# Performance work log

Measured on AMD Instinct MI355X. Metric: run time of the kernel, lower is better.

## Reference

```python
import jax, jax.numpy as jnp
import numpy as np

B, T, NVAR, H, C = 1024, 96, 7, 64, 3  # batch, seq_len/time-points, nvar, ode_hidden, components
H4 = 4 * H


def setup_inputs() -> dict:
    key = jax.random.key(0)
    ks = jax.random.split(key, 12)
    def w(k, shape, fan_in):
        return (jax.random.normal(k, shape, jnp.float32) / np.sqrt(fan_in)).astype(jnp.float32)
    return {
        "x": jax.random.normal(ks[0], (B, T, NVAR), jnp.float32),
        # init_net: Linear(nvar->H), ReLU, Linear(H->C*H)   (stored as (in,out))
        "init_w1": w(ks[1], (NVAR, H), NVAR), "init_b1": jnp.zeros((H,), jnp.float32),
        "init_w2": w(ks[2], (H, C * H), H),   "init_b2": jnp.zeros((C * H,), jnp.float32),
        # ODEFunc.net: Linear(H+C -> 4H), Tanh, Linear(4H -> H)
        "ode_w1": w(ks[3], (H + C, H4), H + C), "ode_b1": jnp.zeros((H4,), jnp.float32),
        "ode_w2": w(ks[4], (H4, H), H4),        "ode_b2": jnp.zeros((H,), jnp.float32),
        # interaction param (init eye) and frozen conservation linear (eye, no bias)
        "interaction": jnp.eye(C, dtype=jnp.float32),
        "conservation": jnp.eye(C, dtype=jnp.float32),
        # decode_net: per-component Linear(H->H), ReLU, Linear(H->nvar)
        "dec_w1": w(ks[5], (C, H, H), H), "dec_b1": jnp.zeros((C, H), jnp.float32),
        "dec_w2": w(ks[6], (C, H, NVAR), H), "dec_b2": jnp.zeros((C, NVAR), jnp.float32),
        "t_points": jnp.linspace(0.0, 1.0, T).astype(jnp.float32),
    }


def _ode_func(t, state, interaction, conservation, ode_w1, ode_b1, ode_w2, ode_b2):
    # state: (B, C, H)
    b = state.shape[0]
    state_comp = state.mean(axis=-1)                                   # (B, C)
    ie = jnp.einsum('ij,bj->bi', interaction, state_comp)              # bmm(interaction, mean)
    ie = jnp.einsum('oi,bi->bo', conservation, ie)                     # frozen linear (no bias)
    inputs = jnp.concatenate(
        [state.reshape(b * C, H), ie.reshape(b * C, 1), jnp.full((b * C, 1), t, state.dtype)],
        axis=1)                                                        # (B*C, H+2)? no: H + 1 + 1 = H + C since C==3? -> H+2; matches torch cat of [H,1,1] only if C accounts: net expects H+C=H+3.
    # NOTE: torch concatenates [state(H), interaction_effect(1), t(1)] = H+2 features but the
    # Linear expects H+C.  With C=3 torch relies on nn.Linear(H+3) receiving H+2?? It does not --
    # torch code passes H+2 features into Linear(H+C).  Faithful translation pads to match below.
    d = jnp.tanh(inputs @ ode_w1[: inputs.shape[1]] + ode_b1) @ ode_w2 + ode_b2
    return d.reshape(state.shape)


def reference(x, init_w1, init_b1, init_w2, init_b2, ode_w1, ode_b1, ode_w2, ode_b2,
              interaction, conservation, dec_w1, dec_b1, dec_w2, dec_b2, t_points):
    # initial state from mean over sequence
    h0 = jax.nn.relu(x.mean(axis=1) @ init_w1 + init_b1)
    y0 = (h0 @ init_w2 + init_b2).reshape(-1, C, H)                    # (B, C, H)

    f = lambda t, y: _ode_func(t, y, interaction, conservation, ode_w1, ode_b1, ode_w2, ode_b2)

    def rk4_step(y, ts):
        t0, t1 = ts
        h = t1 - t0
        k1 = f(t0, y)
        k2 = f(t0 + 0.5 * h, y + 0.5 * h * k1)
        k3 = f(t0 + 0.5 * h, y + 0.5 * h * k2)
        k4 = f(t1, y + h * k3)
        y1 = y + (h / 6.0) * (k1 + 2.0 * k2 + 2.0 * k3 + k4)
        return y1, y1

    ts = jnp.stack([t_points[:-1], t_points[1:]], axis=1)              # (T-1, 2)
    _, ys = jax.lax.scan(rk4_step, y0, ts)                             # (T-1, B, C, H)
    states = jnp.concatenate([y0[None], ys], axis=0)                   # (T, B, C, H)
    states = jnp.transpose(states, (1, 0, 2, 3))                       # (B, T, C, H)

    # per-component decode MLP
    hid = jax.nn.relu(jnp.einsum('btch,chk->btck', states, dec_w1) + dec_b1)
    comps = jnp.einsum('btck,ckn->btcn', hid, dec_w2) + dec_b2         # (B, T, C, NVAR)
    comps = jnp.moveaxis(comps, 2, 0)                                  # (C, B, T, NVAR)
    # comps[0] is the trend, comps[1:] the high-frequency components
    return comps
```

## Files before the change

### kernel.cpp

```cpp
#include <hip/hip_runtime.h>

#define BTOT 1024
#define TPTS 96
#define NV   7
#define HD   64
#define NH   256

typedef short bf16x8 __attribute__((ext_vector_type(8)));
typedef float f32x4  __attribute__((ext_vector_type(4)));
typedef unsigned int u32x4 __attribute__((ext_vector_type(4)));
#define MFMA16(a,b,c) __builtin_amdgcn_mfma_f32_16x16x32_bf16(a,b,c,0,0,0)

#define OFF_YP   0
#define OFF_TP   1024
#define OFF_PRT  5120
#define OFF_YF   7680
#define OFF_PS   8720
#define OFF_TPS  8784
#define OFF_DW1  8880
#define OFF_DW2  21168
#define OFF_DB1  22512
#define OFF_DB2  22704
#define SMEM_WORDS 22736
#define SMEM_BYTES (SMEM_WORDS*4)

__device__ __forceinline__ float rdlane(float v, int i) {
    return __int_as_float(__builtin_amdgcn_readlane(__float_as_int(v), i));
}
__device__ __forceinline__ float wsum64(float v) {
    v += __shfl_xor(v, 1);  v += __shfl_xor(v, 2);  v += __shfl_xor(v, 4);
    v += __shfl_xor(v, 8);  v += __shfl_xor(v, 16); v += __shfl_xor(v, 32);
    return v;
}
__device__ __forceinline__ float tanh_fast(float x) {
    float e = __expf(2.f * x);
    return 1.f - 2.f / (e + 1.f);
}
__device__ __forceinline__ ushort bf16rn(float x) {
    unsigned u = __float_as_uint(x);
    return (ushort)((u + 0x7fffu + ((u >> 16) & 1u)) >> 16);
}
__device__ __forceinline__ void split2(float x, ushort& h, ushort& l) {
    h = bf16rn(x);
    float hf = __uint_as_float(((unsigned)h) << 16);
    l = bf16rn(x - hf);
}

union FU { u32x4 uv; unsigned u[4]; ushort s[8]; bf16x8 v; };

__global__ __launch_bounds__(512, 2)
void node_mfma13(const float* __restrict__ x,
                 const float* __restrict__ iw1, const float* __restrict__ ib1,
                 const float* __restrict__ iw2, const float* __restrict__ ib2,
                 const float* __restrict__ ow1, const float* __restrict__ ob1,
                 const float* __restrict__ ow2, const float* __restrict__ ob2,
                 const float* __restrict__ inter, const float* __restrict__ cons,
                 const float* __restrict__ dw1, const float* __restrict__ db1,
                 const float* __restrict__ dw2, const float* __restrict__ db2,
                 const float* __restrict__ tpts,
                 float* __restrict__ out)
{
    extern __shared__ float sm[];
    unsigned* YPw = (unsigned*)(sm + OFF_YP);
    unsigned* TPw = (unsigned*)(sm + OFF_TP);
    float*    PRT = sm + OFF_PRT;
    float*    Yf  = sm + OFF_YF;
    float*    PS  = sm + OFF_PS;
    float*    tps = sm + OFF_TPS;
    float*    DW1 = sm + OFF_DW1;
    float*    DW2 = sm + OFF_DW2;
    float*    DB1 = sm + OFF_DB1;
    float*    DB2 = sm + OFF_DB2;

    const int tid = threadIdx.x;
    const int w   = tid >> 6;
    const int ln  = tid & 63;
    const int m   = ln & 15;
    const int g4  = ln >> 4;
    const int nt  = w & 3;
    const int kh  = w >> 2;

    for (int idx = tid; idx < 3*HD*HD; idx += 512) DW1[idx] = dw1[idx];
    if (tid < 3*HD)  { for (int v = 0; v < NV; ++v) DW2[tid*NV + v] = dw2[tid*NV + v]; }
    if (tid < 192)   DB1[tid] = db1[tid];
    if (tid < 21)    DB2[tid] = db2[tid];
    if (tid < TPTS)  tps[tid] = tpts[tid];

    FU w1h[2][2], w1l[2][2];
    FU w2h[4], w2l[4];
    #pragma unroll
    for (int u = 0; u < 2; ++u)
        #pragma unroll
        for (int cc = 0; cc < 2; ++cc)
            #pragma unroll
            for (int j = 0; j < 8; ++j) {
                ushort h, l;
                int k1 = 32*cc + 8*g4 + j;
                split2(ow1[k1*NH + 16*(2*w+u) + m], h, l);
                w1h[u][cc].s[j] = h; w1l[u][cc].s[j] = l;
            }
    #pragma unroll
    for (int cc = 0; cc < 4; ++cc)
        #pragma unroll
        for (int j = 0; j < 8; ++j) {
            ushort h, l;
            int k2 = 128*kh + 32*cc + 8*g4 + j;
            split2(ow2[k2*HD + 16*nt + m], h, l);
            w2h[cc].s[j] = h; w2l[cc].s[j] = l;
        }
    float w64c[2], w65c[2], b1c[2];
    #pragma unroll
    for (int u = 0; u < 2; ++u) {
        int c1 = 16*(2*w+u) + m;
        w64c[u] = ow1[64*NH + c1];
        w65c[u] = ow1[65*NH + c1];
        b1c[u]  = ob1[c1];
    }
    const float b2c = ob2[16*nt + m];

    const int cpm = m % 3, base3 = m - cpm;
    float Mr0, Mr1, Mr2;
    {
        float I[9], C[9];
        #pragma unroll
        for (int i = 0; i < 9; ++i) { I[i] = inter[i]; C[i] = cons[i]; }
        float M_[3][3];
        #pragma unroll
        for (int r = 0; r < 3; ++r)
            #pragma unroll
            for (int c = 0; c < 3; ++c)
                M_[r][c] = (C[r*3+0]*I[0*3+c] + C[r*3+1]*I[1*3+c] + C[r*3+2]*I[2*3+c]) * (1.f/64.f);
        Mr0 = (cpm==0) ? M_[0][0] : (cpm==1) ? M_[1][0] : M_[2][0];
        Mr1 = (cpm==0) ? M_[0][1] : (cpm==1) ? M_[1][1] : M_[2][1];
        Mr2 = (cpm==0) ? M_[0][2] : (cpm==1) ? M_[1][2] : M_[2][2];
    }

    {
        const int el0 = w >> 1;
        const int b0  = blockIdx.x*4 + el0;
        float xs0,xs1,xs2,xs3,xs4,xs5,xs6;
        {
            const float* xp = x + (size_t)b0 * TPTS * NV + ln * NV;
            float v0=xp[0],v1=xp[1],v2=xp[2],v3=xp[3],v4=xp[4],v5=xp[5],v6=xp[6];
            if (ln < 32) {
                const float* xp2 = xp + 64 * NV;
                v0+=xp2[0]; v1+=xp2[1]; v2+=xp2[2]; v3+=xp2[3]; v4+=xp2[4]; v5+=xp2[5]; v6+=xp2[6];
            }
            xs0=wsum64(v0)*(1.f/96.f); xs1=wsum64(v1)*(1.f/96.f); xs2=wsum64(v2)*(1.f/96.f);
            xs3=wsum64(v3)*(1.f/96.f); xs4=wsum64(v4)*(1.f/96.f); xs5=wsum64(v5)*(1.f/96.f);
            xs6=wsum64(v6)*(1.f/96.f);
        }
        float h0v;
        {
            float a = ib1[ln];
            a = fmaf(xs0, iw1[0*HD+ln], a); a = fmaf(xs1, iw1[1*HD+ln], a);
            a = fmaf(xs2, iw1[2*HD+ln], a); a = fmaf(xs3, iw1[3*HD+ln], a);
            a = fmaf(xs4, iw1[4*HD+ln], a); a = fmaf(xs5, iw1[5*HD+ln], a);
            a = fmaf(xs6, iw1[6*HD+ln], a);
            h0v = fmaxf(a, 0.f);
        }
        float y0a = ib2[ln], y0b = ib2[64+ln], y0c = ib2[128+ln];
        #pragma unroll
        for (int k = 0; k < 64; ++k) {
            float hk = rdlane(h0v, k);
            y0a = fmaf(hk, iw2[k*192 + ln],       y0a);
            y0b = fmaf(hk, iw2[k*192 + 64 + ln],  y0b);
            y0c = fmaf(hk, iw2[k*192 + 128 + ln], y0c);
        }
        if ((w & 1) == 0) {
            float yv[3] = {y0a, y0b, y0c};
            #pragma unroll
            for (int r = 0; r < 3; ++r) {
                int row = el0*3 + r;
                Yf[row*65 + ln] = yv[r];
                ushort hs, ls; split2(yv[r], hs, ls);
                unsigned hp = hs, lp = ls;
                unsigned hq = __shfl_xor(hp, 1), lq = __shfl_xor(lp, 1);
                if ((ln & 1) == 0) {
                    int wgrp = ln >> 3;
                    int woff = row*32 + ((((unsigned)(wgrp ^ row)) & 7) << 2) + ((ln >> 1) & 3);
                    YPw[woff]       = hp | (hq << 16);
                    YPw[512 + woff] = lp | (lq << 16);
                }
            }
            float S0 = wsum64(y0a), S1 = wsum64(y0b), S2 = wsum64(y0c);
            if (ln < 3) PS[el0*3 + ln] = (ln==0)?S0:(ln==1)?S1:S2;
        }
        if (w == 1 && ln < 48) PS[16 + ln] = 0.f;
        if (w == 5 && ln >= 12 && ln < 16) PS[ln] = 0.f;
        if (w == 3) {
            YPw[384 + ln] = 0u; YPw[448 + ln] = 0u;
            YPw[896 + ln] = 0u; YPw[960 + ln] = 0u;
        }
        if (w == 7) {
            #pragma unroll
            for (int r = 12; r < 16; ++r) Yf[r*65 + ln] = 0.f;
        }
    }
    __syncthreads();

    f32x4 yb, ks;
    #pragma unroll
    for (int r = 0; r < 4; ++r) yb[r] = Yf[(4*g4 + r)*65 + 16*nt + m];

    auto publish = [&](f32x4 ys, bool commit) {
        #pragma unroll
        for (int rr = 0; rr < 2; ++rr) {
            float yv = kh ? (rr ? ys[3] : ys[2]) : (rr ? ys[1] : ys[0]);
            const int row = 4*g4 + 2*kh + rr;
            ushort hs, ls; split2(yv, hs, ls);
            unsigned hp = hs, lp = ls;
            unsigned hq = __shfl_xor(hp, 1), lq = __shfl_xor(lp, 1);
            if ((m & 1) == 0) {
                int wgrp = 2*nt + (m >> 3);
                int woff = row*32 + ((((unsigned)(wgrp ^ row)) & 7) << 2) + ((m >> 1) & 3);
                YPw[woff]       = hp | (hq << 16);
                YPw[512 + woff] = lp | (lq << 16);
            }
            if (commit) Yf[row*65 + 16*nt + m] = yv;
            float s = yv;
            s += __shfl_xor(s, 1); s += __shfl_xor(s, 2);
            s += __shfl_xor(s, 4); s += __shfl_xor(s, 8);
            if (m == 0) PS[nt*16 + row] = s;
        }
    };

    auto evalf = [&](float ts, f32x4& dd) {
        float rsum = (PS[m] + PS[16+m]) + (PS[32+m] + PS[48+m]);
        float eAll = Mr0*__shfl(rsum, base3) + Mr1*__shfl(rsum, base3+1) + Mr2*__shfl(rsum, base3+2);

        f32x4 aA0 = {0,0,0,0}, aB0 = {0,0,0,0}, aA1 = {0,0,0,0}, aB1 = {0,0,0,0};
        #pragma unroll
        for (int cc = 0; cc < 2; ++cc) {
            FU ah, al;
            int aoff = m*32 + ((((unsigned)((4*cc + g4) ^ m)) & 7) << 2);
            ah.uv = *(const u32x4*)(YPw + aoff);
            al.uv = *(const u32x4*)(YPw + 512 + aoff);
            aA0 = MFMA16(ah.v, w1h[0][cc].v, aA0);
            aB0 = MFMA16(ah.v, w1l[0][cc].v, aB0);
            aA0 = MFMA16(al.v, w1h[0][cc].v, aA0);
            aA1 = MFMA16(ah.v, w1h[1][cc].v, aA1);
            aB1 = MFMA16(ah.v, w1l[1][cc].v, aB1);
            aA1 = MFMA16(al.v, w1h[1][cc].v, aA1);
        }
        #pragma unroll
        for (int r = 0; r < 4; ++r) {
            float er = __shfl(eAll, 4*g4 + r);
            const int row = 4*g4 + r;
            #pragma unroll
            for (int u = 0; u < 2; ++u) {
                float val = u ? (aA1[r] + aB1[r]) : (aA0[r] + aB0[r]);
                val = fmaf(w64c[u], er, val);
                val = fmaf(w65c[u], ts, val);
                val += b1c[u];
                float th = tanh_fast(val);
                ushort hs, ls; split2(th, hs, ls);
                unsigned hp = hs, lp = ls;
                unsigned hq = __shfl_xor(hp, 1), lq = __shfl_xor(lp, 1);
                if ((m & 1) == 0) {
                    int wgrp = 4*w + 2*u + (m >> 3);
                    int woff = row*128 + ((((unsigned)wgrp & 24) | (((unsigned)(wgrp ^ row)) & 7)) << 2)
                             + ((m >> 1) & 3);
                    TPw[woff]        = hp | (hq << 16);
                    TPw[2048 + woff] = lp | (lq << 16);
                }
            }
        }
        __syncthreads();

        f32x4 pA = {0,0,0,0}, pB = {0,0,0,0};
        #pragma unroll
        for (int cc = 0; cc < 4; ++cc) {
            FU ah, al;
            int G = 16*kh + 4*cc + g4;
            int aoff = m*128 + ((((unsigned)G & 24) | (((unsigned)(G ^ m)) & 7)) << 2);
            ah.uv = *(const u32x4*)(TPw + aoff);
            al.uv = *(const u32x4*)(TPw + 2048 + aoff);
            pA = MFMA16(ah.v, w2h[cc].v, pA);
            pB = MFMA16(ah.v, w2l[cc].v, pB);
            pA = MFMA16(al.v, w2h[cc].v, pA);
        }
        f32x4 pr = pA + pB;
        *(f32x4*)(PRT + w*320 + m*20 + 4*g4) = pr;
        __syncthreads();

        const float* pb = PRT + m*20 + 4*g4;
        f32x4 q0 = *(const f32x4*)(pb + nt*320);
        f32x4 q1 = *(const f32x4*)(pb + (nt+4)*320);
        f32x4 qq = q0 + q1;
        dd[0] = qq[0] + b2c; dd[1] = qq[1] + b2c;
        dd[2] = qq[2] + b2c; dd[3] = qq[3] + b2c;
    };

    auto decode_row = [&](int row, int tix) {
        const int cc = row % 3, el = row / 3;
        const int b  = blockIdx.x*4 + el;
        float dyv = Yf[row*65 + ln];
        float acc = DB1[cc*HD + ln];
        #pragma unroll 8
        for (int h = 0; h < 64; ++h)
            acc = fmaf(rdlane(dyv, h), DW1[(cc*HD + h)*HD + ln], acc);
        float hid = fmaxf(acc, 0.f);
        #pragma unroll
        for (int v = 0; v < NV; ++v) {
            float pv = wsum64(hid * DW2[(cc*HD + ln)*NV + v]);
            if (ln == 0)
                out[(((size_t)cc*BTOT + b)*TPTS + tix)*NV + v] = pv + DB2[cc*NV + v];
        }
    };
    auto decode = [&](int tix) {
        decode_row(w, tix);
        if (w < 4) decode_row(w + 8, tix);
    };

    decode(0);
    f32x4 dd;
    #pragma unroll 1
    for (int s = 0; s < TPTS - 1; ++s) {
        const float ta = tps[s], tb = tps[s + 1];
        const float dt = tb - ta, hdt = 0.5f * dt;

        evalf(ta, dd);
        ks = dd; publish(yb + hdt*dd, false);
        __syncthreads();

        evalf(ta + hdt, dd);
        ks += 2.f*dd; publish(yb + hdt*dd, false);
        __syncthreads();

        evalf(ta + hdt, dd);
        ks += 2.f*dd; publish(yb + dt*dd, false);
        __syncthreads();

        evalf(tb, dd);
        ks += dd; yb = yb + (dt*(1.f/6.f))*ks; publish(yb, true);
        __syncthreads();

        decode(s + 1);
    }
}

extern "C" void kernel_launch(void* const* d_in, const int* in_sizes, int n_in,
                              void* d_out, int out_size, void* d_ws, size_t ws_size,
                              hipStream_t stream) {
    const float* x     = (const float*)d_in[0];
    const float* iw1   = (const float*)d_in[1];
    const float* ib1   = (const float*)d_in[2];
    const float* iw2   = (const float*)d_in[3];
    const float* ib2   = (const float*)d_in[4];
    const float* ow1   = (const float*)d_in[5];
    const float* ob1   = (const float*)d_in[6];
    const float* ow2   = (const float*)d_in[7];
    const float* ob2   = (const float*)d_in[8];
    const float* inter = (const float*)d_in[9];
    const float* cons  = (const float*)d_in[10];
    const float* dw1   = (const float*)d_in[11];
    const float* db1   = (const float*)d_in[12];
    const float* dw2   = (const float*)d_in[13];
    const float* db2   = (const float*)d_in[14];
    const float* tpts  = (const float*)d_in[15];
    float* out = (float*)d_out;

    (void)hipFuncSetAttribute((const void*)node_mfma13,
                              hipFuncAttributeMaxDynamicSharedMemorySize,
                              SMEM_BYTES);

    node_mfma13<<<BTOT / 4, 512, SMEM_BYTES, stream>>>(
        x, iw1, ib1, iw2, ib2, ow1, ob1, ow2, ob2,
        inter, cons, dw1, db1, dw2, db2, tpts, out);
}
```

Before: 1.326 ms.

## Drop split-K partial reduction in second ODE GEMM, stream low weights from LDS

The second ODE layer GEMM is no longer split over K between wave pairs. Each wave now computes the full K=256 reduction for its output tile and writes no partial sums. This removes the PRT scratch buffer, a __syncthreads and an LDS round-trip on every function evaluation. To keep register pressure in check, only the high bf16 halves of W2 stay in registers; the low halves move into a swizzled LDS array read each step. The cost is duplicated MFMA work across waves (8 waves doing 4 tiles' worth each twice), more LDS traffic and larger shared memory, which may lower occupancy.

After: 1.416 ms. 6.8% more time.

```diff
diff --git a/kernel.cpp b/kernel.cpp
--- a/kernel.cpp
+++ b/kernel.cpp
@@ -11,17 +11,17 @@
 typedef unsigned int u32x4 __attribute__((ext_vector_type(4)));
 #define MFMA16(a,b,c) __builtin_amdgcn_mfma_f32_16x16x32_bf16(a,b,c,0,0,0)
 
-#define OFF_YP   0
-#define OFF_TP   1024
-#define OFF_PRT  5120
-#define OFF_YF   7680
-#define OFF_PS   8720
-#define OFF_TPS  8784
-#define OFF_DW1  8880
-#define OFF_DW2  21168
-#define OFF_DB1  22512
-#define OFF_DB2  22704
-#define SMEM_WORDS 22736
+#define OFF_YP    0
+#define OFF_TP    1024
+#define OFF_W2LO  5120
+#define OFF_YF    13312
+#define OFF_PS    14352
+#define OFF_TPS   14416
+#define OFF_DW1   14512
+#define OFF_DW2   26800
+#define OFF_DB1   28144
+#define OFF_DB2   28336
+#define SMEM_WORDS 28368
 #define SMEM_BYTES (SMEM_WORDS*4)
 
 __device__ __forceinline__ float rdlane(float v, int i) {
@@ -49,7 +49,7 @@
 union FU { u32x4 uv; unsigned u[4]; ushort s[8]; bf16x8 v; };
 
 __global__ __launch_bounds__(512, 2)
-void node_mfma13(const float* __restrict__ x,
+void node_mfma14(const float* __restrict__ x,
                  const float* __restrict__ iw1, const float* __restrict__ ib1,
                  const float* __restrict__ iw2, const float* __restrict__ ib2,
                  const float* __restrict__ ow1, const float* __restrict__ ob1,
@@ -63,7 +63,7 @@
     extern __shared__ float sm[];
     unsigned* YPw = (unsigned*)(sm + OFF_YP);
     unsigned* TPw = (unsigned*)(sm + OFF_TP);
-    float*    PRT = sm + OFF_PRT;
+    unsigned* W2L = (unsigned*)(sm + OFF_W2LO);
     float*    Yf  = sm + OFF_YF;
     float*    PS  = sm + OFF_PS;
     float*    tps = sm + OFF_TPS;
@@ -86,8 +86,19 @@
     if (tid < 21)    DB2[tid] = db2[tid];
     if (tid < TPTS)  tps[tid] = tpts[tid];
 
+    {
+        ushort* W2Lu = (ushort*)W2L;
+        for (int idx = tid; idx < NH*HD; idx += 512) {
+            int k = idx >> 6, o = idx & 63;
+            ushort h, l; split2(ow2[idx], h, l);
+            int gi = k >> 3;
+            int word = o*128 + ((((unsigned)(gi ^ (o & 31))) & 31) << 2) + ((k >> 1) & 3);
+            W2Lu[word*2 + (k & 1)] = l;
+        }
+    }
+
     FU w1h[2][2], w1l[2][2];
-    FU w2h[4], w2l[4];
+    FU w2h[8];
     #pragma unroll
     for (int u = 0; u < 2; ++u)
         #pragma unroll
@@ -100,13 +111,13 @@
                 w1h[u][cc].s[j] = h; w1l[u][cc].s[j] = l;
             }
     #pragma unroll
-    for (int cc = 0; cc < 4; ++cc)
+    for (int cc = 0; cc < 8; ++cc)
         #pragma unroll
         for (int j = 0; j < 8; ++j) {
             ushort h, l;
-            int k2 = 128*kh + 32*cc + 8*g4 + j;
+            int k2 = 32*cc + 8*g4 + j;
             split2(ow2[k2*HD + 16*nt + m], h, l);
-            w2h[cc].s[j] = h; w2l[cc].s[j] = l;
+            w2h[cc].s[j] = h;
         }
     float w64c[2], w65c[2], b1c[2];
     #pragma unroll
@@ -269,25 +280,21 @@
         __syncthreads();
 
         f32x4 pA = {0,0,0,0}, pB = {0,0,0,0};
-        #pragma unroll
-        for (int cc = 0; cc < 4; ++cc) {
-            FU ah, al;
-            int G = 16*kh + 4*cc + g4;
+        const int o = 16*nt + m;
+        #pragma unroll
+        for (int cc = 0; cc < 8; ++cc) {
+            FU ah, al, bl;
+            int G = 4*cc + g4;
             int aoff = m*128 + ((((unsigned)G & 24) | (((unsigned)(G ^ m)) & 7)) << 2);
             ah.uv = *(const u32x4*)(TPw + aoff);
             al.uv = *(const u32x4*)(TPw + 2048 + aoff);
+            int woff = o*128 + ((((unsigned)(G ^ (o & 31))) & 31) << 2);
+            bl.uv = *(const u32x4*)(W2L + woff);
             pA = MFMA16(ah.v, w2h[cc].v, pA);
-            pB = MFMA16(ah.v, w2l[cc].v, pB);
+            pB = MFMA16(ah.v, bl.v, pB);
             pA = MFMA16(al.v, w2h[cc].v, pA);
         }
-        f32x4 pr = pA + pB;
-        *(f32x4*)(PRT + w*320 + m*20 + 4*g4) = pr;
-        __syncthreads();
-
-        const float* pb = PRT + m*20 + 4*g4;
-        f32x4 q0 = *(const f32x4*)(pb + nt*320);
-        f32x4 q1 = *(const f32x4*)(pb + (nt+4)*320);
-        f32x4 qq = q0 + q1;
+        f32x4 qq = pA + pB;
         dd[0] = qq[0] + b2c; dd[1] = qq[1] + b2c;
         dd[2] = qq[2] + b2c; dd[3] = qq[3] + b2c;
     };
@@ -361,11 +368,11 @@
     const float* tpts  = (const float*)d_in[15];
     float* out = (float*)d_out;
 
-    (void)hipFuncSetAttribute((const void*)node_mfma13,
+    (void)hipFuncSetAttribute((const void*)node_mfma14,
                               hipFuncAttributeMaxDynamicSharedMemorySize,
                               SMEM_BYTES);
 
-    node_mfma13<<<BTOT / 4, 512, SMEM_BYTES, stream>>>(
+    node_mfma14<<<BTOT / 4, 512, SMEM_BYTES, stream>>>(
         x, iw1, ib1, iw2, ib2, ow1, ob1, ow2, ob2,
         inter, cons, dw1, db1, dw2, db2, tpts, out);
 }
```
